# Optimization experiments

Measured on AMD Instinct MI355X. Metric: run time of the kernel, lower is better.

The kernel has to match this reference:

```python
import jax, jax.numpy as jnp
import numpy as np


def setup_inputs() -> dict:
    key = jax.random.key(0)
    k1, k2, k3 = jax.random.split(key, 3)
    B, N, Nq, D, Dv = 32, 4096, 8, 64, 64
    return {
        "keys": jax.random.normal(k1, (B, N, D), dtype=jnp.float32),
        "values": jax.random.normal(k2, (B, N, Dv), dtype=jnp.float32),
        "query": jax.random.normal(k3, (B, Nq, D), dtype=jnp.float32),
    }


def reference(keys, values, query):
    eps = 1e-8
    d = keys.shape[-1]
    # scores: B x N x N'  (same math as broadcast multiply + sum over D)
    alpha = jnp.einsum("bnd,bmd->bnm", keys, query) / jnp.sqrt(jnp.float32(d))
    # softmax over slots (last axis)
    alpha = jax.nn.softmax(alpha, axis=-1) + eps
    # renormalize over input tokens (axis=1)
    alpha = alpha / jnp.sum(alpha, axis=1, keepdims=True)
    # weighted sum of values over N: B x N' x D'
    return jnp.einsum("bnm,bnv->bmv", alpha, values)
```

## Files before the change

kernel.cpp:

```cpp
#include <hip/hip_runtime.h>

#define BB 32
#define NN 4096
#define NQ 8
#define DD 64
#define DV 64
#define CHUNKS 16
#define TOK_PER_BLOCK (NN / CHUNKS)
#define TOK_PER_WAVE (TOK_PER_BLOCK / 4)
#define BATCH 4
#define NBATCH (TOK_PER_WAVE / BATCH)

__global__ __launch_bounds__(256, 2) void slot_attn_partial(
    const float* __restrict__ keys, const float* __restrict__ values,
    const float* __restrict__ query, float* __restrict__ PU, float* __restrict__ PS)
{
    const int b    = blockIdx.y;
    const int chnk = blockIdx.x;
    const int tid  = threadIdx.x;
    const int wave = tid >> 6;
    const int lane = tid & 63;
    const int m    = lane >> 3;
    const int g    = lane & 7;

    const float4* qp = (const float4*)(query + ((size_t)b * NQ + m) * DD + 8 * g);
    const float4 q0 = qp[0];
    const float4 q1 = qp[1];

    const float* Kbase = keys   + (size_t)b * NN * DD + 8 * g;
    const float* Vbase = values + (size_t)b * NN * DV + 8 * g;

    float u[8];
#pragma unroll
    for (int j = 0; j < 8; ++j) u[j] = 0.f;
    float s_acc = 0.f;

    const int tok0 = chnk * TOK_PER_BLOCK + wave * TOK_PER_WAVE;

    float4 K0[2][BATCH], K1[2][BATCH], V0[2][BATCH], V1[2][BATCH];

    auto load_batch = [&](int buf, int t0) {
#pragma unroll
        for (int uu = 0; uu < BATCH; ++uu) {
            const float4* kp = (const float4*)(Kbase + (size_t)(t0 + uu) * DD);
            const float4* vp = (const float4*)(Vbase + (size_t)(t0 + uu) * DV);
            K0[buf][uu] = kp[0]; K1[buf][uu] = kp[1];
            V0[buf][uu] = vp[0]; V1[buf][uu] = vp[1];
        }
    };

    auto compute_batch = [&](int buf) {
#pragma unroll
        for (int uu = 0; uu < BATCH; ++uu) {
            const float4 k0 = K0[buf][uu], k1 = K1[buf][uu];
            float s = k0.x * q0.x + k0.y * q0.y + k0.z * q0.z + k0.w * q0.w
                    + k1.x * q1.x + k1.y * q1.y + k1.z * q1.z + k1.w * q1.w;
            s += __shfl_xor(s, 1, 64);
            s += __shfl_xor(s, 2, 64);
            s += __shfl_xor(s, 4, 64);
            s *= 0.125f;
            float e = __expf(s);
            float sm = e;
            sm += __shfl_xor(sm, 8, 64);
            sm += __shfl_xor(sm, 16, 64);
            sm += __shfl_xor(sm, 32, 64);
            const float alpha = e * __builtin_amdgcn_rcpf(sm) + 1e-8f;
            s_acc += alpha;
            const float4 v0 = V0[buf][uu], v1 = V1[buf][uu];
            u[0] += alpha * v0.x;
            u[1] += alpha * v0.y;
            u[2] += alpha * v0.z;
            u[3] += alpha * v0.w;
            u[4] += alpha * v1.x;
            u[5] += alpha * v1.y;
            u[6] += alpha * v1.z;
            u[7] += alpha * v1.w;
        }
    };

    load_batch(0, tok0);
#pragma unroll
    for (int i = 0; i < NBATCH; ++i) {
        const int cur = i & 1;
        if (i + 1 < NBATCH) load_batch(cur ^ 1, tok0 + (i + 1) * BATCH);
        compute_batch(cur);
    }

    __shared__ float lds[4 * 512];
    __shared__ float lds_s[4 * 8];
    float* dst = lds + wave * 512 + m * 64 + 8 * g;
#pragma unroll
    for (int j = 0; j < 8; ++j) dst[j] = u[j];
    if (g == 0) lds_s[wave * 8 + m] = s_acc;
    __syncthreads();

    float* pu = PU + ((size_t)b * CHUNKS + chnk) * 512;
#pragma unroll
    for (int o = 0; o < 2; ++o) {
        int idx = o * 256 + tid;
        pu[idx] = lds[idx] + lds[512 + idx] + lds[1024 + idx] + lds[1536 + idx];
    }
    if (tid < 8) {
        PS[((size_t)b * CHUNKS + chnk) * 8 + tid] =
            lds_s[tid] + lds_s[8 + tid] + lds_s[16 + tid] + lds_s[24 + tid];
    }
}

__global__ __launch_bounds__(512) void slot_attn_reduce(
    const float* __restrict__ PU, const float* __restrict__ PS,
    float* __restrict__ out)
{
    const int b = blockIdx.x;
    const int i = threadIdx.x;

    __shared__ float ssum[NQ];
    if (i < NQ) {
        float s = 0.f;
        const float* ps = PS + (size_t)b * CHUNKS * 8 + i;
#pragma unroll
        for (int c = 0; c < CHUNKS; ++c) s += ps[c * 8];
        ssum[i] = s;
    }
    __syncthreads();

    float usum = 0.f;
    const float* pu = PU + (size_t)b * CHUNKS * 512 + i;
#pragma unroll
    for (int c = 0; c < CHUNKS; ++c) usum += pu[c * 512];
    out[(size_t)b * 512 + i] = usum / ssum[i >> 6];
}

extern "C" void kernel_launch(void* const* d_in, const int* in_sizes, int n_in,
                              void* d_out, int out_size, void* d_ws, size_t ws_size,
                              hipStream_t stream) {
    const float* keys   = (const float*)d_in[0];
    const float* values = (const float*)d_in[1];
    const float* query  = (const float*)d_in[2];
    float* out = (float*)d_out;

    float* PU = (float*)d_ws;
    float* PS = PU + (size_t)BB * CHUNKS * 512;

    slot_attn_partial<<<dim3(CHUNKS, BB), 256, 0, stream>>>(keys, values, query, PU, PS);
    slot_attn_reduce<<<dim3(BB), 512, 0, stream>>>(PU, PS, out);
}
```

Measured before the change: 120.1 us.

## Remap lanes to tokens so each lane loads K/V once for all slots

Each 8-lane group now handles a distinct token and computes all 8 slot scores itself. Before, the 8 slot groups in a wave each re-loaded the same token's K/V from memory. The softmax over slots becomes a per-lane sum with a single reciprocal instead of cross-lane shuffles. A cross-token shuffle reduction runs at the end before the LDS write. The cost is heavy register pressure (64 accumulators plus 16 query float4s) under a launch bound of two blocks per CU, which risks spills or lower occupancy.

```diff
diff --git a/kernel.cpp b/kernel.cpp
--- a/kernel.cpp
+++ b/kernel.cpp
@@ -8,90 +8,110 @@
 #define CHUNKS 16
 #define TOK_PER_BLOCK (NN / CHUNKS)
 #define TOK_PER_WAVE (TOK_PER_BLOCK / 4)
-#define BATCH 4
-#define NBATCH (TOK_PER_WAVE / BATCH)
+#define NGROUP (TOK_PER_WAVE / 8)
 
 __global__ __launch_bounds__(256, 2) void slot_attn_partial(
     const float* __restrict__ keys, const float* __restrict__ values,
     const float* __restrict__ query, float* __restrict__ PU, float* __restrict__ PS)
 {
-    const int b    = blockIdx.y;
-    const int chnk = blockIdx.x;
-    const int tid  = threadIdx.x;
-    const int wave = tid >> 6;
-    const int lane = tid & 63;
-    const int m    = lane >> 3;
-    const int g    = lane & 7;
+    const int b     = blockIdx.y;
+    const int chnk  = blockIdx.x;
+    const int tid   = threadIdx.x;
+    const int wave  = tid >> 6;
+    const int lane  = tid & 63;
+    const int t_sub = lane >> 3;
+    const int g     = lane & 7;
 
-    const float4* qp = (const float4*)(query + ((size_t)b * NQ + m) * DD + 8 * g);
-    const float4 q0 = qp[0];
-    const float4 q1 = qp[1];
+    float4 q0[8], q1[8];
+    const float* qb = query + (size_t)b * NQ * DD + 8 * g;
+#pragma unroll
+    for (int m = 0; m < 8; ++m) {
+        q0[m] = *(const float4*)(qb + m * DD);
+        q1[m] = *(const float4*)(qb + m * DD + 4);
+    }
 
     const float* Kbase = keys   + (size_t)b * NN * DD + 8 * g;
     const float* Vbase = values + (size_t)b * NN * DV + 8 * g;
 
-    float u[8];
+    float u[8][8];
 #pragma unroll
-    for (int j = 0; j < 8; ++j) u[j] = 0.f;
-    float s_acc = 0.f;
+    for (int m = 0; m < 8; ++m)
+#pragma unroll
+        for (int j = 0; j < 8; ++j) u[m][j] = 0.f;
+    float s_acc[8];
+#pragma unroll
+    for (int m = 0; m < 8; ++m) s_acc[m] = 0.f;
 
     const int tok0 = chnk * TOK_PER_BLOCK + wave * TOK_PER_WAVE;
 
-    float4 K0[2][BATCH], K1[2][BATCH], V0[2][BATCH], V1[2][BATCH];
+    const float4* kp = (const float4*)(Kbase + (size_t)(tok0 + t_sub) * DD);
+    const float4* vp = (const float4*)(Vbase + (size_t)(tok0 + t_sub) * DV);
+    float4 kc0 = kp[0], kc1 = kp[1], vc0 = vp[0], vc1 = vp[1];
 
-    auto load_batch = [&](int buf, int t0) {
 #pragma unroll
-        for (int uu = 0; uu < BATCH; ++uu) {
-            const float4* kp = (const float4*)(Kbase + (size_t)(t0 + uu) * DD);
-            const float4* vp = (const float4*)(Vbase + (size_t)(t0 + uu) * DV);
-            K0[buf][uu] = kp[0]; K1[buf][uu] = kp[1];
-            V0[buf][uu] = vp[0]; V1[buf][uu] = vp[1];
+    for (int i = 0; i < NGROUP; ++i) {
+        float4 kn0, kn1, vn0, vn1;
+        if (i + 1 < NGROUP) {
+            const float4* kq = (const float4*)(Kbase + (size_t)(tok0 + 8 * (i + 1) + t_sub) * DD);
+            const float4* vq = (const float4*)(Vbase + (size_t)(tok0 + 8 * (i + 1) + t_sub) * DV);
+            kn0 = kq[0]; kn1 = kq[1]; vn0 = vq[0]; vn1 = vq[1];
         }
-    };
 
-    auto compute_batch = [&](int buf) {
+        float s[8];
 #pragma unroll
-        for (int uu = 0; uu < BATCH; ++uu) {
-            const float4 k0 = K0[buf][uu], k1 = K1[buf][uu];
-            float s = k0.x * q0.x + k0.y * q0.y + k0.z * q0.z + k0.w * q0.w
-                    + k1.x * q1.x + k1.y * q1.y + k1.z * q1.z + k1.w * q1.w;
-            s += __shfl_xor(s, 1, 64);
-            s += __shfl_xor(s, 2, 64);
-            s += __shfl_xor(s, 4, 64);
-            s *= 0.125f;
-            float e = __expf(s);
-            float sm = e;
-            sm += __shfl_xor(sm, 8, 64);
-            sm += __shfl_xor(sm, 16, 64);
-            sm += __shfl_xor(sm, 32, 64);
-            const float alpha = e * __builtin_amdgcn_rcpf(sm) + 1e-8f;
-            s_acc += alpha;
-            const float4 v0 = V0[buf][uu], v1 = V1[buf][uu];
-            u[0] += alpha * v0.x;
-            u[1] += alpha * v0.y;
-            u[2] += alpha * v0.z;
-            u[3] += alpha * v0.w;
-            u[4] += alpha * v1.x;
-            u[5] += alpha * v1.y;
-            u[6] += alpha * v1.z;
-            u[7] += alpha * v1.w;
+        for (int m = 0; m < 8; ++m) {
+            s[m] = kc0.x * q0[m].x + kc0.y * q0[m].y + kc0.z * q0[m].z + kc0.w * q0[m].w
+                 + kc1.x * q1[m].x + kc1.y * q1[m].y + kc1.z * q1[m].z + kc1.w * q1[m].w;
         }
-    };
+#pragma unroll
+        for (int m = 0; m < 8; ++m) {
+            s[m] += __shfl_xor(s[m], 1, 64);
+            s[m] += __shfl_xor(s[m], 2, 64);
+            s[m] += __shfl_xor(s[m], 4, 64);
+        }
+        float e[8], sum = 0.f;
+#pragma unroll
+        for (int m = 0; m < 8; ++m) { e[m] = __expf(s[m] * 0.125f); sum += e[m]; }
+        const float r = __builtin_amdgcn_rcpf(sum);
+#pragma unroll
+        for (int m = 0; m < 8; ++m) {
+            const float a = e[m] * r + 1e-8f;
+            s_acc[m] += a;
+            u[m][0] += a * vc0.x; u[m][1] += a * vc0.y;
+            u[m][2] += a * vc0.z; u[m][3] += a * vc0.w;
+            u[m][4] += a * vc1.x; u[m][5] += a * vc1.y;
+            u[m][6] += a * vc1.z; u[m][7] += a * vc1.w;
+        }
 
-    load_batch(0, tok0);
+        if (i + 1 < NGROUP) { kc0 = kn0; kc1 = kn1; vc0 = vn0; vc1 = vn1; }
+    }
+
 #pragma unroll
-    for (int i = 0; i < NBATCH; ++i) {
-        const int cur = i & 1;
-        if (i + 1 < NBATCH) load_batch(cur ^ 1, tok0 + (i + 1) * BATCH);
-        compute_batch(cur);
+    for (int m = 0; m < 8; ++m) {
+#pragma unroll
+        for (int j = 0; j < 8; ++j) {
+            u[m][j] += __shfl_xor(u[m][j], 8, 64);
+            u[m][j] += __shfl_xor(u[m][j], 16, 64);
+            u[m][j] += __shfl_xor(u[m][j], 32, 64);
+        }
+        s_acc[m] += __shfl_xor(s_acc[m], 8, 64);
+        s_acc[m] += __shfl_xor(s_acc[m], 16, 64);
+        s_acc[m] += __shfl_xor(s_acc[m], 32, 64);
     }
 
     __shared__ float lds[4 * 512];
     __shared__ float lds_s[4 * 8];
-    float* dst = lds + wave * 512 + m * 64 + 8 * g;
+    if (t_sub == 0) {
+        float* dst = lds + wave * 512 + 8 * g;
 #pragma unroll
-    for (int j = 0; j < 8; ++j) dst[j] = u[j];
-    if (g == 0) lds_s[wave * 8 + m] = s_acc;
+        for (int m = 0; m < 8; ++m)
+#pragma unroll
+            for (int j = 0; j < 8; ++j) dst[m * 64 + j] = u[m][j];
+        if (g == 0) {
+#pragma unroll
+            for (int m = 0; m < 8; ++m) lds_s[wave * 8 + m] = s_acc[m];
+        }
+    }
     __syncthreads();
 
     float* pu = PU + ((size_t)b * CHUNKS + chnk) * 512;
```

After: 107.3 us. 10.6% less time.
